# Kernel tuning notes

Hardware: AMD Instinct MI355X
Metric: run time of the kernel (lower is better)

The kernel has to match this reference:

```python
import jax, jax.numpy as jnp
import numpy as np
from functools import partial

SUBJECT_CATEGORY_ID = 0
PNMS_THRESH = 0.7


def box_cxcywh_to_xyxy(b):
    cx, cy, w, h = jnp.split(b, 4, axis=-1)
    return jnp.concatenate([cx - 0.5 * w, cy - 0.5 * h, cx + 0.5 * w, cy + 0.5 * h], axis=-1)


def box_iou(b1, b2):
    # b1: [Q,4], b2: [Q,4] (xyxy) -> [Q,Q] IoU (torchvision-style)
    area1 = (b1[:, 2] - b1[:, 0]) * (b1[:, 3] - b1[:, 1])
    area2 = (b2[:, 2] - b2[:, 0]) * (b2[:, 3] - b2[:, 1])
    lt = jnp.maximum(b1[:, None, :2], b2[None, :, :2])
    rb = jnp.minimum(b1[:, None, 2:], b2[None, :, 2:])
    wh = jnp.clip(rb - lt, 0.0)
    inter = wh[..., 0] * wh[..., 1]
    union = area1[:, None] + area2[None, :] - inter
    return inter / union


def pnms_one(vs, ol, pair_iou):
    # vs: [Q,V] verb scores, ol: [Q] int labels, pair_iou: [Q,Q].
    # Replicates the original greedy per-class suppression, including the
    # original's row-i update vs[i, suppressed_queries] -= 1 (requires Q <= V).
    Q, V = vs.shape

    def class_step(vs, i):
        col = jnp.take(vs, i, axis=1)           # [Q]
        order = jnp.argsort(-col)               # descending, like reversed argsort

        def greedy(carry, j):
            alive, supp = carry
            is_alive = alive[j]
            kill = alive & (ol == ol[j]) & (pair_iou[j] > PNMS_THRESH)
            kill = kill.at[j].set(False)
            kill = kill & is_alive
            alive_next = (alive & ~kill).at[j].set(False)
            alive = jnp.where(is_alive, alive_next, alive)
            return (alive, supp | kill), None

        (alive, supp), _ = jax.lax.scan(
            greedy, (jnp.ones((Q,), bool), jnp.zeros((Q,), bool)), order)
        delta = jnp.zeros((V,), vs.dtype).at[:Q].set(supp.astype(vs.dtype))
        vs = vs.at[i].add(-delta)
        return vs, None

    vs, _ = jax.lax.scan(class_step, vs, jnp.arange(V))
    return vs


def setup_inputs() -> dict:
    key = jax.random.key(0)
    k1, k2, k3, k4, k5 = jax.random.split(key, 5)
    B, Q, C, V = 1024, 100, 81, 117
    return {
        'obj_logits': jax.random.normal(k1, (B, Q, C), jnp.float32),
        'verb_logits': jax.random.normal(k2, (B, Q, V), jnp.float32),
        'sub_boxes': jax.random.uniform(k3, (B, Q, 4), jnp.float32),
        'obj_boxes': jax.random.uniform(k4, (B, Q, 4), jnp.float32),
        'target_sizes': jax.random.randint(k5, (B, 2), 0, 1333, jnp.int32),
    }


def reference(obj_logits, verb_logits, sub_boxes, obj_boxes, target_sizes):
    obj_prob = jax.nn.softmax(obj_logits, axis=-1)
    obj_scores = obj_prob[..., :-1].max(-1)                 # [B,Q]
    obj_labels = jnp.argmax(obj_prob[..., :-1], axis=-1)    # [B,Q]
    verb_scores = jax.nn.sigmoid(verb_logits)               # [B,Q,V]

    sizes = target_sizes.astype(jnp.float32)
    img_h, img_w = sizes[:, 0], sizes[:, 1]
    scale = jnp.stack([img_w, img_h, img_w, img_h], axis=1)  # [B,4]
    sb = box_cxcywh_to_xyxy(sub_boxes) * scale[:, None, :]
    ob = box_cxcywh_to_xyxy(obj_boxes) * scale[:, None, :]

    sub_labels = jnp.full_like(obj_labels, SUBJECT_CATEGORY_ID)
    labels = jnp.concatenate([sub_labels, obj_labels], axis=1)   # [B,2Q]
    boxes = jnp.concatenate([sb, ob], axis=1)                    # [B,2Q,4]

    vs = verb_scores * obj_scores[..., None]                     # [B,Q,V]
    pair_iou = jnp.minimum(jax.vmap(box_iou)(sb, sb), jax.vmap(box_iou)(ob, ob))
    vs = jax.vmap(pnms_one)(vs, obj_labels, pair_iou)
    return vs, obj_scores, labels, boxes
```

## Files before the change

### kernel.cpp

```cpp
#include <hip/hip_runtime.h>
#include <math.h>

#define Q 100
#define NC 81
#define NV 117
#define MAXK 48
#define NV4 2925

__global__ __launch_bounds__(512) void hoi_fused(
    const float*  __restrict__ obj_logits,
    const float4* __restrict__ verb4,
    const float*  __restrict__ sub_boxes,
    const float*  __restrict__ obj_boxes,
    const int*    __restrict__ target_sizes,
    float* __restrict__ out_vs,
    float* __restrict__ out_scores,
    float* __restrict__ out_labels,
    float* __restrict__ out_boxes)
{
    __shared__ float  score_s[Q];
    __shared__ int    labi[Q];
    __shared__ float4 sb4[Q], ob4[Q];
    __shared__ float  area_s[Q], area_o[Q];
    __shared__ unsigned long long lbl_bits[NC - 1][2];
    __shared__ unsigned long long mask_s[2 * Q];
    __shared__ unsigned long long killset_s[2 * Q];
    __shared__ int   clist_s[Q];
    __shared__ float col_s[Q];
    __shared__ float vsrow[MAXK * 101];
    __shared__ int   anyconf, Ksh;

    const int b    = blockIdx.x;
    const int tid  = threadIdx.x;
    const int lane = tid & 63;
    const int sl   = lane & 15;
    const int r16  = tid >> 4;

    if (tid == 0) anyconf = 0;
    if (tid < 2 * Q) killset_s[tid] = 0ull;
    if (tid < 2 * (NC - 1)) ((unsigned long long*)lbl_bits)[tid] = 0ull;

    for (int qi = r16; qi < Q; qi += 32) {
        const float* lp = obj_logits + ((size_t)b * Q + qi) * NC;
        float v[5];
        #pragma unroll
        for (int c = 0; c < 5; ++c) v[c] = lp[sl + c * 16];
        const float l80 = lp[80];

        float bv = v[0]; int bi = sl;
        #pragma unroll
        for (int c = 1; c < 5; ++c)
            if (v[c] > bv) { bv = v[c]; bi = sl + c * 16; }
        #pragma unroll
        for (int d = 1; d < 16; d <<= 1) {
            float ov = __shfl_xor(bv, d, 16);
            int   oi = __shfl_xor(bi, d, 16);
            if (ov > bv || (ov == bv && oi < bi)) { bv = ov; bi = oi; }
        }
        const float m = fmaxf(bv, l80);

        float s = (sl == 0) ? __expf(l80 - m) : 0.f;
        #pragma unroll
        for (int c = 0; c < 5; ++c) s += __expf(v[c] - m);
        #pragma unroll
        for (int d = 1; d < 16; d <<= 1) s += __shfl_xor(s, d, 16);

        if (sl == 0) {
            score_s[qi] = __fmul_rn(__expf(bv - m), __builtin_amdgcn_rcpf(s));
            labi[qi] = bi;
        }
    }
    __syncthreads();

    if (tid < 2 * Q) {
        const int q = (tid < Q) ? tid : tid - Q;
        const float fh = (float)target_sizes[2 * b];
        const float fw = (float)target_sizes[2 * b + 1];
        const float4* src = reinterpret_cast<const float4*>(tid < Q ? sub_boxes : obj_boxes);
        float4 cxy = src[(size_t)b * Q + q];
        float hw = __fmul_rn(0.5f, cxy.z);
        float hh = __fmul_rn(0.5f, cxy.w);
        float4 box;
        box.x = __fmul_rn(__fsub_rn(cxy.x, hw), fw);
        box.y = __fmul_rn(__fsub_rn(cxy.y, hh), fh);
        box.z = __fmul_rn(__fadd_rn(cxy.x, hw), fw);
        box.w = __fmul_rn(__fadd_rn(cxy.y, hh), fh);
        float area = __fmul_rn(__fsub_rn(box.z, box.x), __fsub_rn(box.w, box.y));
        if (tid < Q) { sb4[q] = box; area_s[q] = area; }
        else         { ob4[q] = box; area_o[q] = area; }
        reinterpret_cast<float4*>(out_boxes)[(size_t)b * 2 * Q + tid] = box;
        out_labels[(size_t)b * 2 * Q + tid] = (tid < Q) ? 0.0f : (float)labi[q];
    }
    if (tid < Q) {
        out_scores[(size_t)b * Q + tid] = score_s[tid];
        atomicOr(&lbl_bits[labi[tid]][tid >> 6], 1ull << (tid & 63));
    }

    {
        const size_t base4 = (size_t)b * NV4;
        float4* ovs4 = reinterpret_cast<float4*>(out_vs);
        for (int idx = tid; idx < NV4; idx += 512) {
            float4 x = verb4[base4 + idx];
            float xv[4] = {x.x, x.y, x.z, x.w};
            float r[4];
            #pragma unroll
            for (int j = 0; j < 4; ++j) {
                int lq = (idx * 4 + j) / NV;
                float sg = __builtin_amdgcn_rcpf(__fadd_rn(1.0f, __expf(-xv[j])));
                r[j] = __fmul_rn(sg, score_s[lq]);
            }
            ovs4[base4 + idx] = make_float4(r[0], r[1], r[2], r[3]);
        }
    }
    __syncthreads();

    if (tid < Q) {
        const int j = tid;
        const float4 sj = sb4[j]; const float asj = area_s[j];
        const float4 oj = ob4[j]; const float aoj = area_o[j];
        const int lj = labi[j];
        unsigned long long bits[2] = {0ull, 0ull};
        #pragma unroll
        for (int w = 0; w < 2; ++w) {
            unsigned long long mm = lbl_bits[lj][w];
            if (w == (j >> 6)) mm &= ~(1ull << (j & 63));
            while (mm) {
                int kb = __builtin_ctzll(mm); mm &= mm - 1;
                int k = kb + w * 64;
                float4 sk = sb4[k];
                float wx = fmaxf(__fsub_rn(fminf(sj.z, sk.z), fmaxf(sj.x, sk.x)), 0.f);
                float wy = fmaxf(__fsub_rn(fminf(sj.w, sk.w), fmaxf(sj.y, sk.y)), 0.f);
                float inter = __fmul_rn(wx, wy);
                float uni = __fsub_rn(__fadd_rn(asj, area_s[k]), inter);
                float ious = __fdiv_rn(inter, uni);
                float4 ok = ob4[k];
                wx = fmaxf(__fsub_rn(fminf(oj.z, ok.z), fmaxf(oj.x, ok.x)), 0.f);
                wy = fmaxf(__fsub_rn(fminf(oj.w, ok.w), fmaxf(oj.y, ok.y)), 0.f);
                inter = __fmul_rn(wx, wy);
                uni = __fsub_rn(__fadd_rn(aoj, area_o[k]), inter);
                float iouo = __fdiv_rn(inter, uni);
                if (ious != ious || iouo != iouo) continue;
                if (fminf(ious, iouo) > 0.7f) bits[w] |= 1ull << kb;
            }
        }
        mask_s[2 * j]     = bits[0];
        mask_s[2 * j + 1] = bits[1];
        if (bits[0] | bits[1]) anyconf = 1;
    }
    __syncthreads();

    if (!anyconf) return;

    if (tid == 0) {
        int K = 0;
        for (int q = 0; q < Q; ++q)
            if (mask_s[2 * q] | mask_s[2 * q + 1]) clist_s[K++] = q;
        Ksh = K;
    }
    __syncthreads();
    const int K = Ksh;
    const bool staged = (K <= MAXK);

    if (staged) {
        for (int idx = tid; idx < K * Q; idx += 512) {
            int k = idx / Q, i = idx - k * Q;
            vsrow[k * 101 + i] = out_vs[(size_t)b * Q * NV + clist_s[k] * NV + i];
        }
    }
    __syncthreads();

    if (tid == 0) {
        for (int i = 0; i < Q; ++i) {
            for (int k = 0; k < K; ++k) {
                int c = clist_s[k];
                float v = staged ? vsrow[k * 101 + i]
                                 : out_vs[(size_t)b * Q * NV + c * NV + i];
                if ((killset_s[2 * c + (i >> 6)] >> (i & 63)) & 1ull)
                    v = __fsub_rn(v, 1.0f);
                col_s[k] = v;
            }
            unsigned long long alive0 = ~0ull, alive1 = (1ull << 36) - 1;
            unsigned long long supp0 = 0ull, supp1 = 0ull;
            for (int t = 0; t < K; ++t) {
                float best = col_s[0]; int bk = 0;
                for (int k = 1; k < K; ++k) { float ck = col_s[k]; if (ck > best) { best = ck; bk = k; } }
                col_s[bk] = -3.0e38f;
                int q = clist_s[bk];
                bool al = (q < 64) ? ((alive0 >> q) & 1ull) : ((alive1 >> (q - 64)) & 1ull);
                if (al) {
                    unsigned long long m0 = mask_s[2 * q], m1 = mask_s[2 * q + 1];
                    supp0 |= alive0 & m0;
                    supp1 |= alive1 & m1;
                    alive0 &= ~m0;
                    alive1 &= ~m1;
                    if (q < 64) alive0 &= ~(1ull << q); else alive1 &= ~(1ull << (q - 64));
                }
            }
            killset_s[2 * i]     = supp0;
            killset_s[2 * i + 1] = supp1;
        }
    }
    __syncthreads();

    for (int idx = tid; idx < Q * Q; idx += 512) {
        int qrow = idx / Q, v = idx - qrow * Q;
        if ((killset_s[2 * qrow + (v >> 6)] >> (v & 63)) & 1ull) {
            size_t a = (size_t)b * Q * NV + qrow * NV + v;
            out_vs[a] = __fsub_rn(out_vs[a], 1.0f);
        }
    }
}

extern "C" void kernel_launch(void* const* d_in, const int* in_sizes, int n_in,
                              void* d_out, int out_size, void* d_ws, size_t ws_size,
                              hipStream_t stream) {
    const float* obj_logits   = (const float*)d_in[0];
    const float* verb_logits  = (const float*)d_in[1];
    const float* sub_boxes    = (const float*)d_in[2];
    const float* obj_boxes    = (const float*)d_in[3];
    const int*   target_sizes = (const int*)d_in[4];
    const int B  = in_sizes[0] / (Q * NC);

    float* out_vs     = (float*)d_out;
    float* out_scores = out_vs + (size_t)B * Q * NV;
    float* out_labels = out_scores + (size_t)B * Q;
    float* out_boxes  = out_labels + (size_t)B * 2 * Q;

    hoi_fused<<<dim3(B), dim3(512), 0, stream>>>(
        obj_logits, (const float4*)verb_logits,
        sub_boxes, obj_boxes, target_sizes,
        out_vs, out_scores, out_labels, out_boxes);
}
```

Before: 131.0 us.

## Split into prep kernel computing kill masks and streaming verb-score kernel

The single fused kernel becomes two. The first computes scores, labels, boxes, the pair-IoU conflict masks and the greedy suppression kill sets, and writes those bitmasks to workspace. For staged rows it recomputes sigmoid scores directly from the logits instead of re-reading out_vs. The second kernel streams verb logits once, applying sigmoid, score scaling and the -1 suppression in a single write, which removes the read-modify-write pass over out_vs. The cost is an extra launch and a workspace round trip, and the streaming kernel cannot start until the serial greedy phase has finished for all blocks.

```diff
diff --git a/kernel.cpp b/kernel.cpp
--- a/kernel.cpp
+++ b/kernel.cpp
@@ -6,17 +6,18 @@
 #define NV 117
 #define MAXK 48
 #define NV4 2925
-
-__global__ __launch_bounds__(512) void hoi_fused(
+#define WSB 202
+
+__global__ __launch_bounds__(512) void k_prep(
     const float*  __restrict__ obj_logits,
-    const float4* __restrict__ verb4,
+    const float*  __restrict__ verb_logits,
     const float*  __restrict__ sub_boxes,
     const float*  __restrict__ obj_boxes,
     const int*    __restrict__ target_sizes,
-    float* __restrict__ out_vs,
     float* __restrict__ out_scores,
     float* __restrict__ out_labels,
-    float* __restrict__ out_boxes)
+    float* __restrict__ out_boxes,
+    unsigned long long* __restrict__ wsk)
 {
     __shared__ float  score_s[Q];
     __shared__ int    labi[Q];
@@ -25,6 +26,7 @@
     __shared__ unsigned long long lbl_bits[NC - 1][2];
     __shared__ unsigned long long mask_s[2 * Q];
     __shared__ unsigned long long killset_s[2 * Q];
+    __shared__ unsigned long long krow_s[2];
     __shared__ int   clist_s[Q];
     __shared__ float col_s[Q];
     __shared__ float vsrow[MAXK * 101];
@@ -32,11 +34,10 @@
 
     const int b    = blockIdx.x;
     const int tid  = threadIdx.x;
-    const int lane = tid & 63;
-    const int sl   = lane & 15;
+    const int sl   = tid & 15;
     const int r16  = tid >> 4;
 
-    if (tid == 0) anyconf = 0;
+    if (tid == 0) { anyconf = 0; krow_s[0] = 0ull; krow_s[1] = 0ull; }
     if (tid < 2 * Q) killset_s[tid] = 0ull;
     if (tid < 2 * (NC - 1)) ((unsigned long long*)lbl_bits)[tid] = 0ull;
 
@@ -94,23 +95,6 @@
     if (tid < Q) {
         out_scores[(size_t)b * Q + tid] = score_s[tid];
         atomicOr(&lbl_bits[labi[tid]][tid >> 6], 1ull << (tid & 63));
-    }
-
-    {
-        const size_t base4 = (size_t)b * NV4;
-        float4* ovs4 = reinterpret_cast<float4*>(out_vs);
-        for (int idx = tid; idx < NV4; idx += 512) {
-            float4 x = verb4[base4 + idx];
-            float xv[4] = {x.x, x.y, x.z, x.w};
-            float r[4];
-            #pragma unroll
-            for (int j = 0; j < 4; ++j) {
-                int lq = (idx * 4 + j) / NV;
-                float sg = __builtin_amdgcn_rcpf(__fadd_rn(1.0f, __expf(-xv[j])));
-                r[j] = __fmul_rn(sg, score_s[lq]);
-            }
-            ovs4[base4 + idx] = make_float4(r[0], r[1], r[2], r[3]);
-        }
     }
     __syncthreads();
 
@@ -149,65 +133,135 @@
     }
     __syncthreads();
 
-    if (!anyconf) return;
-
-    if (tid == 0) {
-        int K = 0;
-        for (int q = 0; q < Q; ++q)
-            if (mask_s[2 * q] | mask_s[2 * q + 1]) clist_s[K++] = q;
-        Ksh = K;
-    }
-    __syncthreads();
-    const int K = Ksh;
-    const bool staged = (K <= MAXK);
-
-    if (staged) {
-        for (int idx = tid; idx < K * Q; idx += 512) {
-            int k = idx / Q, i = idx - k * Q;
-            vsrow[k * 101 + i] = out_vs[(size_t)b * Q * NV + clist_s[k] * NV + i];
-        }
-    }
-    __syncthreads();
-
-    if (tid == 0) {
-        for (int i = 0; i < Q; ++i) {
-            for (int k = 0; k < K; ++k) {
+    if (anyconf) {
+        if (tid == 0) {
+            int K = 0;
+            for (int q = 0; q < Q; ++q)
+                if (mask_s[2 * q] | mask_s[2 * q + 1]) clist_s[K++] = q;
+            Ksh = K;
+        }
+        __syncthreads();
+        const int K = Ksh;
+        const bool staged = (K <= MAXK);
+
+        if (staged) {
+            for (int idx = tid; idx < K * Q; idx += 512) {
+                int k = idx / Q, i = idx - k * Q;
                 int c = clist_s[k];
-                float v = staged ? vsrow[k * 101 + i]
-                                 : out_vs[(size_t)b * Q * NV + c * NV + i];
-                if ((killset_s[2 * c + (i >> 6)] >> (i & 63)) & 1ull)
-                    v = __fsub_rn(v, 1.0f);
-                col_s[k] = v;
-            }
-            unsigned long long alive0 = ~0ull, alive1 = (1ull << 36) - 1;
-            unsigned long long supp0 = 0ull, supp1 = 0ull;
-            for (int t = 0; t < K; ++t) {
-                float best = col_s[0]; int bk = 0;
-                for (int k = 1; k < K; ++k) { float ck = col_s[k]; if (ck > best) { best = ck; bk = k; } }
-                col_s[bk] = -3.0e38f;
-                int q = clist_s[bk];
-                bool al = (q < 64) ? ((alive0 >> q) & 1ull) : ((alive1 >> (q - 64)) & 1ull);
-                if (al) {
-                    unsigned long long m0 = mask_s[2 * q], m1 = mask_s[2 * q + 1];
-                    supp0 |= alive0 & m0;
-                    supp1 |= alive1 & m1;
-                    alive0 &= ~m0;
-                    alive1 &= ~m1;
-                    if (q < 64) alive0 &= ~(1ull << q); else alive1 &= ~(1ull << (q - 64));
-                }
-            }
-            killset_s[2 * i]     = supp0;
-            killset_s[2 * i + 1] = supp1;
-        }
-    }
-    __syncthreads();
-
-    for (int idx = tid; idx < Q * Q; idx += 512) {
-        int qrow = idx / Q, v = idx - qrow * Q;
-        if ((killset_s[2 * qrow + (v >> 6)] >> (v & 63)) & 1ull) {
-            size_t a = (size_t)b * Q * NV + qrow * NV + v;
-            out_vs[a] = __fsub_rn(out_vs[a], 1.0f);
-        }
+                float x = verb_logits[(size_t)b * Q * NV + c * NV + i];
+                float sg = __builtin_amdgcn_rcpf(__fadd_rn(1.0f, __expf(-x)));
+                vsrow[k * 101 + i] = __fmul_rn(sg, score_s[c]);
+            }
+        }
+        __syncthreads();
+
+        if (tid == 0) {
+            for (int i = 0; i < Q; ++i) {
+                for (int k = 0; k < K; ++k) {
+                    int c = clist_s[k];
+                    float v;
+                    if (staged) v = vsrow[k * 101 + i];
+                    else {
+                        float x = verb_logits[(size_t)b * Q * NV + c * NV + i];
+                        float sg = __builtin_amdgcn_rcpf(__fadd_rn(1.0f, __expf(-x)));
+                        v = __fmul_rn(sg, score_s[c]);
+                    }
+                    if ((killset_s[2 * c + (i >> 6)] >> (i & 63)) & 1ull)
+                        v = __fsub_rn(v, 1.0f);
+                    col_s[k] = v;
+                }
+                unsigned long long alive0 = ~0ull, alive1 = (1ull << 36) - 1;
+                unsigned long long supp0 = 0ull, supp1 = 0ull;
+                for (int t = 0; t < K; ++t) {
+                    float best = col_s[0]; int bk = 0;
+                    for (int k = 1; k < K; ++k) { float ck = col_s[k]; if (ck > best) { best = ck; bk = k; } }
+                    col_s[bk] = -3.0e38f;
+                    int q = clist_s[bk];
+                    bool al = (q < 64) ? ((alive0 >> q) & 1ull) : ((alive1 >> (q - 64)) & 1ull);
+                    if (al) {
+                        unsigned long long m0 = mask_s[2 * q], m1 = mask_s[2 * q + 1];
+                        supp0 |= alive0 & m0;
+                        supp1 |= alive1 & m1;
+                        alive0 &= ~m0;
+                        alive1 &= ~m1;
+                        if (q < 64) alive0 &= ~(1ull << q); else alive1 &= ~(1ull << (q - 64));
+                    }
+                }
+                killset_s[2 * i]     = supp0;
+                killset_s[2 * i + 1] = supp1;
+            }
+            unsigned long long kr0 = 0ull, kr1 = 0ull;
+            for (int i = 0; i < Q; ++i)
+                if (killset_s[2 * i] | killset_s[2 * i + 1]) {
+                    if (i < 64) kr0 |= 1ull << i; else kr1 |= 1ull << (i - 64);
+                }
+            krow_s[0] = kr0; krow_s[1] = kr1;
+        }
+        __syncthreads();
+    }
+
+    if (tid < WSB)
+        wsk[(size_t)b * WSB + tid] = (tid < 2 * Q) ? killset_s[tid] : krow_s[tid - 2 * Q];
+}
+
+__global__ __launch_bounds__(512) void k_stream(
+    const float4* __restrict__ verb4,
+    const float*  __restrict__ scores,
+    const unsigned long long* __restrict__ wsk,
+    float4* __restrict__ out4)
+{
+    __shared__ float score_l[Q];
+    __shared__ unsigned long long killset_l[2 * Q];
+
+    const int b   = blockIdx.x;
+    const int tid = threadIdx.x;
+
+    if (tid < Q) score_l[tid] = scores[(size_t)b * Q + tid];
+    const unsigned long long kr0 = wsk[(size_t)b * WSB + 200];
+    const unsigned long long kr1 = wsk[(size_t)b * WSB + 201];
+    const bool anykill = (kr0 | kr1) != 0ull;
+    if (anykill && tid < 2 * Q)
+        killset_l[tid] = wsk[(size_t)b * WSB + tid];
+    __syncthreads();
+
+    const size_t base4 = (size_t)b * NV4;
+    for (int r = tid; r < NV4; r += 512) {
+        float4 x = verb4[base4 + r];
+        const int e  = r * 4;
+        const int q0 = (unsigned)e / 117u;
+        const int q3 = (unsigned)(e + 3) / 117u;
+        float o[4];
+        float xv[4] = {x.x, x.y, x.z, x.w};
+        if (q0 == q3) {
+            const float sc = score_l[q0];
+            #pragma unroll
+            for (int j = 0; j < 4; ++j) {
+                float sg = __builtin_amdgcn_rcpf(__fadd_rn(1.0f, __expf(-xv[j])));
+                o[j] = __fmul_rn(sg, sc);
+            }
+            if (anykill && ((q0 < 64 ? (kr0 >> q0) : (kr1 >> (q0 - 64))) & 1ull)) {
+                const int v0 = e - q0 * 117;
+                #pragma unroll
+                for (int j = 0; j < 4; ++j) {
+                    int v = v0 + j;
+                    if ((killset_l[2 * q0 + (v >> 6)] >> (v & 63)) & 1ull)
+                        o[j] = __fsub_rn(o[j], 1.0f);
+                }
+            }
+        } else {
+            #pragma unroll
+            for (int j = 0; j < 4; ++j) {
+                int ej = e + j;
+                int qj = (unsigned)ej / 117u;
+                int vj = ej - qj * 117;
+                float sg = __builtin_amdgcn_rcpf(__fadd_rn(1.0f, __expf(-xv[j])));
+                o[j] = __fmul_rn(sg, score_l[qj]);
+                if (anykill && ((qj < 64 ? (kr0 >> qj) : (kr1 >> (qj - 64))) & 1ull))
+                    if ((killset_l[2 * qj + (vj >> 6)] >> (vj & 63)) & 1ull)
+                        o[j] = __fsub_rn(o[j], 1.0f);
+            }
+        }
+        out4[base4 + r] = make_float4(o[0], o[1], o[2], o[3]);
     }
 }
 
@@ -225,9 +279,12 @@
     float* out_scores = out_vs + (size_t)B * Q * NV;
     float* out_labels = out_scores + (size_t)B * Q;
     float* out_boxes  = out_labels + (size_t)B * 2 * Q;
-
-    hoi_fused<<<dim3(B), dim3(512), 0, stream>>>(
-        obj_logits, (const float4*)verb_logits,
-        sub_boxes, obj_boxes, target_sizes,
-        out_vs, out_scores, out_labels, out_boxes);
+    unsigned long long* wsk = (unsigned long long*)d_ws;
+
+    k_prep<<<dim3(B), dim3(512), 0, stream>>>(
+        obj_logits, verb_logits, sub_boxes, obj_boxes, target_sizes,
+        out_scores, out_labels, out_boxes, wsk);
+
+    k_stream<<<dim3(B), dim3(512), 0, stream>>>(
+        (const float4*)verb_logits, out_scores, wsk, (float4*)out_vs);
 }
```

New measurement: 137.7 us. 5.1% more time.

## Defer verb score write until after suppression to avoid out_vs read-modify-write

Applied to the files above, without the earlier changes.

Moves the sigmoid-times-score write of out_vs to the end of the kernel and folds the per-entry suppression subtract into that single pass. The staged rows for conflicting queries are now recomputed from verb_logits instead of being read back from out_vs. This removes the global re-read and rewrite of out_vs entries during suppression. In exchange, the streaming write now waits until after the serial single-thread NMS loop, so it no longer overlaps with it.

```diff
diff --git a/kernel.cpp b/kernel.cpp
--- a/kernel.cpp
+++ b/kernel.cpp
@@ -9,7 +9,7 @@
 
 __global__ __launch_bounds__(512) void hoi_fused(
     const float*  __restrict__ obj_logits,
-    const float4* __restrict__ verb4,
+    const float*  __restrict__ verb_logits,
     const float*  __restrict__ sub_boxes,
     const float*  __restrict__ obj_boxes,
     const int*    __restrict__ target_sizes,
@@ -32,8 +32,7 @@
 
     const int b    = blockIdx.x;
     const int tid  = threadIdx.x;
-    const int lane = tid & 63;
-    const int sl   = lane & 15;
+    const int sl   = tid & 15;
     const int r16  = tid >> 4;
 
     if (tid == 0) anyconf = 0;
@@ -94,23 +93,6 @@
     if (tid < Q) {
         out_scores[(size_t)b * Q + tid] = score_s[tid];
         atomicOr(&lbl_bits[labi[tid]][tid >> 6], 1ull << (tid & 63));
-    }
-
-    {
-        const size_t base4 = (size_t)b * NV4;
-        float4* ovs4 = reinterpret_cast<float4*>(out_vs);
-        for (int idx = tid; idx < NV4; idx += 512) {
-            float4 x = verb4[base4 + idx];
-            float xv[4] = {x.x, x.y, x.z, x.w};
-            float r[4];
-            #pragma unroll
-            for (int j = 0; j < 4; ++j) {
-                int lq = (idx * 4 + j) / NV;
-                float sg = __builtin_amdgcn_rcpf(__fadd_rn(1.0f, __expf(-xv[j])));
-                r[j] = __fmul_rn(sg, score_s[lq]);
-            }
-            ovs4[base4 + idx] = make_float4(r[0], r[1], r[2], r[3]);
-        }
     }
     __syncthreads();
 
@@ -149,64 +131,90 @@
     }
     __syncthreads();
 
-    if (!anyconf) return;
-
-    if (tid == 0) {
-        int K = 0;
-        for (int q = 0; q < Q; ++q)
-            if (mask_s[2 * q] | mask_s[2 * q + 1]) clist_s[K++] = q;
-        Ksh = K;
-    }
-    __syncthreads();
-    const int K = Ksh;
-    const bool staged = (K <= MAXK);
-
-    if (staged) {
-        for (int idx = tid; idx < K * Q; idx += 512) {
-            int k = idx / Q, i = idx - k * Q;
-            vsrow[k * 101 + i] = out_vs[(size_t)b * Q * NV + clist_s[k] * NV + i];
-        }
-    }
-    __syncthreads();
-
-    if (tid == 0) {
-        for (int i = 0; i < Q; ++i) {
-            for (int k = 0; k < K; ++k) {
+    if (anyconf) {
+        if (tid == 0) {
+            int K = 0;
+            for (int q = 0; q < Q; ++q)
+                if (mask_s[2 * q] | mask_s[2 * q + 1]) clist_s[K++] = q;
+            Ksh = K;
+        }
+        __syncthreads();
+        const int K = Ksh;
+        const bool staged = (K <= MAXK);
+
+        if (staged) {
+            for (int idx = tid; idx < K * Q; idx += 512) {
+                int k = idx / Q, i = idx - k * Q;
                 int c = clist_s[k];
-                float v = staged ? vsrow[k * 101 + i]
-                                 : out_vs[(size_t)b * Q * NV + c * NV + i];
-                if ((killset_s[2 * c + (i >> 6)] >> (i & 63)) & 1ull)
-                    v = __fsub_rn(v, 1.0f);
-                col_s[k] = v;
-            }
-            unsigned long long alive0 = ~0ull, alive1 = (1ull << 36) - 1;
-            unsigned long long supp0 = 0ull, supp1 = 0ull;
-            for (int t = 0; t < K; ++t) {
-                float best = col_s[0]; int bk = 0;
-                for (int k = 1; k < K; ++k) { float ck = col_s[k]; if (ck > best) { best = ck; bk = k; } }
-                col_s[bk] = -3.0e38f;
-                int q = clist_s[bk];
-                bool al = (q < 64) ? ((alive0 >> q) & 1ull) : ((alive1 >> (q - 64)) & 1ull);
-                if (al) {
-                    unsigned long long m0 = mask_s[2 * q], m1 = mask_s[2 * q + 1];
-                    supp0 |= alive0 & m0;
-                    supp1 |= alive1 & m1;
-                    alive0 &= ~m0;
-                    alive1 &= ~m1;
-                    if (q < 64) alive0 &= ~(1ull << q); else alive1 &= ~(1ull << (q - 64));
+                float x = verb_logits[(size_t)b * Q * NV + c * NV + i];
+                float sg = __builtin_amdgcn_rcpf(__fadd_rn(1.0f, __expf(-x)));
+                vsrow[k * 101 + i] = __fmul_rn(sg, score_s[c]);
+            }
+        }
+        __syncthreads();
+
+        if (tid == 0) {
+            for (int i = 0; i < Q; ++i) {
+                for (int k = 0; k < K; ++k) {
+                    int c = clist_s[k];
+                    float v;
+                    if (staged) v = vsrow[k * 101 + i];
+                    else {
+                        float x = verb_logits[(size_t)b * Q * NV + c * NV + i];
+                        float sg = __builtin_amdgcn_rcpf(__fadd_rn(1.0f, __expf(-x)));
+                        v = __fmul_rn(sg, score_s[c]);
+                    }
+                    if ((killset_s[2 * c + (i >> 6)] >> (i & 63)) & 1ull)
+                        v = __fsub_rn(v, 1.0f);
+                    col_s[k] = v;
                 }
-            }
-            killset_s[2 * i]     = supp0;
-            killset_s[2 * i + 1] = supp1;
-        }
-    }
-    __syncthreads();
-
-    for (int idx = tid; idx < Q * Q; idx += 512) {
-        int qrow = idx / Q, v = idx - qrow * Q;
-        if ((killset_s[2 * qrow + (v >> 6)] >> (v & 63)) & 1ull) {
-            size_t a = (size_t)b * Q * NV + qrow * NV + v;
-            out_vs[a] = __fsub_rn(out_vs[a], 1.0f);
+                unsigned long long alive0 = ~0ull, alive1 = (1ull << 36) - 1;
+                unsigned long long supp0 = 0ull, supp1 = 0ull;
+                for (int t = 0; t < K; ++t) {
+                    float best = col_s[0]; int bk = 0;
+                    for (int k = 1; k < K; ++k) { float ck = col_s[k]; if (ck > best) { best = ck; bk = k; } }
+                    col_s[bk] = -3.0e38f;
+                    int q = clist_s[bk];
+                    bool al = (q < 64) ? ((alive0 >> q) & 1ull) : ((alive1 >> (q - 64)) & 1ull);
+                    if (al) {
+                        unsigned long long m0 = mask_s[2 * q], m1 = mask_s[2 * q + 1];
+                        supp0 |= alive0 & m0;
+                        supp1 |= alive1 & m1;
+                        alive0 &= ~m0;
+                        alive1 &= ~m1;
+                        if (q < 64) alive0 &= ~(1ull << q); else alive1 &= ~(1ull << (q - 64));
+                    }
+                }
+                killset_s[2 * i]     = supp0;
+                killset_s[2 * i + 1] = supp1;
+            }
+        }
+        __syncthreads();
+    }
+
+    {
+        const size_t base4 = (size_t)b * NV4;
+        const float4* v4 = reinterpret_cast<const float4*>(verb_logits);
+        float4* ovs4 = reinterpret_cast<float4*>(out_vs);
+        const bool kills = anyconf;
+        for (int r = tid; r < NV4; r += 512) {
+            float4 x = v4[base4 + r];
+            const int e = r * 4;
+            float xv[4] = {x.x, x.y, x.z, x.w};
+            float o[4];
+            #pragma unroll
+            for (int j = 0; j < 4; ++j) {
+                int ej = e + j;
+                int qj = (unsigned)ej / 117u;
+                float sg = __builtin_amdgcn_rcpf(__fadd_rn(1.0f, __expf(-xv[j])));
+                o[j] = __fmul_rn(sg, score_s[qj]);
+                if (kills) {
+                    int vj = ej - qj * 117;
+                    if ((killset_s[2 * qj + (vj >> 6)] >> (vj & 63)) & 1ull)
+                        o[j] = __fsub_rn(o[j], 1.0f);
+                }
+            }
+            ovs4[base4 + r] = make_float4(o[0], o[1], o[2], o[3]);
         }
     }
 }
@@ -227,7 +235,6 @@
     float* out_boxes  = out_labels + (size_t)B * 2 * Q;
 
     hoi_fused<<<dim3(B), dim3(512), 0, stream>>>(
-        obj_logits, (const float4*)verb_logits,
-        sub_boxes, obj_boxes, target_sizes,
+        obj_logits, verb_logits, sub_boxes, obj_boxes, target_sizes,
         out_vs, out_scores, out_labels, out_boxes);
 }
```

Result: slower. 134.2 us (+2.5%).
